# Optimization experiments

Measured on AMD Instinct MI355X. Metric: run time of the kernel, lower is better.

Reference implementation:

```python
import jax, jax.numpy as jnp
import numpy as np

H = 4                      # attention heads
L_NAMES = ['self', 'cross'] * 3
K_LIST = [None, None, 128, 128, 64, 64]  # top-k per layer (None = full attention)
BN_EPS = 1e-5


def conv1d(x, W, b):
    # 1x1 Conv1d: x [B, Ci, N], W [Co, Ci], b [Co]
    return jnp.einsum('oi,bin->bon', W, x) + b[:, None]


def bn_eval(x, g, b):
    # BatchNorm1d in eval mode with running mean 0 / var 1
    inv = 1.0 / np.sqrt(1.0 + BN_EPS)
    return (g * inv)[:, None] * x + b[:, None]


def mha(x, src, Wq, bq, Wk, bk, Wv, bv, Wm, bm, k):
    B, D, N = x.shape
    dh = D // H
    q = conv1d(x, Wq, bq).reshape(B, dh, H, N)
    kk = conv1d(src, Wk, bk).reshape(B, dh, H, -1)
    v = conv1d(src, Wv, bv).reshape(B, dh, H, -1)
    scores = jnp.einsum('bdhn,bdhm->bhnm', q, kk) / np.sqrt(dh)  # [B,H,N,M]
    if k is None:
        p = jax.nn.softmax(scores, axis=-1)
        out = jnp.einsum('bhnm,bdhm->bdhn', p, v)
    else:
        vals, idx = jax.lax.top_k(scores, k)          # [B,H,N,k]
        S = jax.nn.softmax(vals, axis=-1)
        # gather value vectors at the top-k key indices: [B,dh,H,N,k]
        vg = jnp.take_along_axis(v[:, :, :, None, :], idx[:, None, :, :, :], axis=4)
        out = jnp.einsum('bhnk,bdhnk->bdhn', S, vg)
    return conv1d(out.reshape(B, D, N), Wm, bm)


def log_ot(scores, alpha, iters):
    b, m, n = scores.shape
    bins0 = jnp.broadcast_to(alpha, (b, m, 1))
    bins1 = jnp.broadcast_to(alpha, (b, 1, n))
    a = jnp.broadcast_to(alpha, (b, 1, 1))
    Z0 = jnp.concatenate([jnp.concatenate([scores, bins0], -1),
                          jnp.concatenate([bins1, a], -1)], 1)  # [b,m+1,n+1]
    norm = -np.log(float(m + n))
    log_mu = jnp.concatenate([jnp.full((m,), norm, scores.dtype),
                              jnp.array([np.log(float(n)) + norm], scores.dtype)])
    log_nu = jnp.concatenate([jnp.full((n,), norm, scores.dtype),
                              jnp.array([np.log(float(m)) + norm], scores.dtype)])
    log_mu = jnp.broadcast_to(log_mu, (b, m + 1))
    log_nu = jnp.broadcast_to(log_nu, (b, n + 1))

    def step(carry, _):
        u, v = carry
        u = log_mu - jax.nn.logsumexp(Z0 + v[:, None, :], axis=2)
        v = log_nu - jax.nn.logsumexp(Z0 + u[:, :, None], axis=1)
        return (u, v), None

    (u, v), _ = jax.lax.scan(step, (jnp.zeros_like(log_mu), jnp.zeros_like(log_nu)),
                             None, length=iters)
    return Z0 + u[:, :, None] + v[:, None, :] - norm


def _forward(desc0, desc1, Wq, bq, Wk, bk, Wv, bv, Wm, bm,
             W1, b1, g1, be1, W2, b2, Wf, bf, alpha, iters):
    d0, d1 = desc0, desc1
    for i, (name, k) in enumerate(zip(L_NAMES, K_LIST)):
        s0, s1 = (d1, d0) if name == 'cross' else (d0, d1)

        def prop(x, src):
            msg = mha(x, src, Wq[i], bq[i], Wk[i], bk[i], Wv[i], bv[i], Wm[i], bm[i], k)
            h = jnp.concatenate([x, msg], axis=1)           # [B, 2D, N]
            h = jax.nn.relu(bn_eval(conv1d(h, W1[i], b1[i]), g1[i], be1[i]))
            return conv1d(h, W2[i], b2[i])

        dlt0, dlt1 = prop(d0, s0), prop(d1, s1)
        d0, d1 = d0 + dlt0, d1 + dlt1
    m0 = conv1d(d0, Wf, bf)
    m1 = conv1d(d1, Wf, bf)
    scores = jnp.einsum('bdn,bdm->bnm', m0, m1) / np.sqrt(m0.shape[1])
    return log_ot(scores, alpha, iters)


def setup_inputs() -> dict:
    B, D, N, L = 4, 128, 1024, 6
    key = jax.random.key(0)
    ks = jax.random.split(key, 20)

    def nrm(k, shape, s):
        return jax.random.normal(k, shape, jnp.float32) * s

    sw = 1.0 / np.sqrt(D)
    return {
        'desc0': nrm(ks[0], (B, D, N), 1.0),
        'desc1': nrm(ks[1], (B, D, N), 1.0),
        'Wq': nrm(ks[2], (L, D, D), sw), 'bq': jnp.zeros((L, D), jnp.float32),
        'Wk': nrm(ks[3], (L, D, D), sw), 'bk': jnp.zeros((L, D), jnp.float32),
        'Wv': nrm(ks[4], (L, D, D), sw), 'bv': jnp.zeros((L, D), jnp.float32),
        'Wm': nrm(ks[5], (L, D, D), sw), 'bm': jnp.zeros((L, D), jnp.float32),
        'W1': nrm(ks[6], (L, 2 * D, 2 * D), 1.0 / np.sqrt(2 * D)),
        'b1': jnp.zeros((L, 2 * D), jnp.float32),
        'g1': jnp.ones((L, 2 * D), jnp.float32),
        'be1': jnp.zeros((L, 2 * D), jnp.float32),
        'W2': nrm(ks[7], (L, D, 2 * D), 1.0 / np.sqrt(2 * D)),
        'b2': jnp.zeros((L, D), jnp.float32),
        'Wf': nrm(ks[8], (D, D), sw), 'bf': jnp.zeros((D,), jnp.float32),
        'alpha': jnp.asarray(1.0, jnp.float32),
        'iters': 20,
    }


def reference(desc0, desc1, Wq, bq, Wk, bk, Wv, bv, Wm, bm,
              W1, b1, g1, be1, W2, b2, Wf, bf, alpha, iters):
    return _forward(desc0, desc1, Wq, bq, Wk, bk, Wv, bv, Wm, bm,
                    W1, b1, g1, be1, W2, b2, Wf, bf, alpha, iters)
```

## Files before the change

### kernel.cpp

```cpp
#include <hip/hip_runtime.h>
#include <hip/hip_fp16.h>
#include <stdint.h>

#define NPOS   1024
#define DMODEL 128
#define NP1    1025
#define PLP    1053700
#define PSTR   1028
#define PLPH   1057800
#define PSTRH  1032
#define NORMF  (-7.624618986159398f)
#define LOGN   (6.931471805599453f)

typedef __attribute__((ext_vector_type(8))) short s8v;
typedef __attribute__((ext_vector_type(4))) float f4v;
typedef unsigned short ushort_t;

#define MFMA(a, b, c) __builtin_amdgcn_mfma_f32_16x16x32_bf16((a), (b), (c), 0, 0, 0)

static __device__ __forceinline__ ushort_t f2bf(float f) {
    union { float f; uint32_t u; } c; c.f = f;
    uint32_t u = c.u;
    return (ushort_t)((u + 0x7fffu + ((u >> 16) & 1u)) >> 16);
}
static __device__ __forceinline__ uint32_t cvtpk(float lo, float hi) {
    uint32_t r;
    asm("v_cvt_pk_bf16_f32 %0, %1, %2" : "=v"(r) : "v"(lo), "v"(hi));
    return r;
}

#define NW0 294912
#define NW1 98304
#define NW2 393216
#define NW3 196608
#define NW4 16384
#define NB5 2304
__global__ __launch_bounds__(256) void prep_weights(
    const float* __restrict__ Wq, const float* __restrict__ Wk, const float* __restrict__ Wv,
    const float* __restrict__ bq, const float* __restrict__ bk, const float* __restrict__ bv,
    const float* __restrict__ Wm, const float* __restrict__ W1, const float* __restrict__ W2,
    const float* __restrict__ Wf,
    ushort_t* __restrict__ wqkv, ushort_t* __restrict__ wm, ushort_t* __restrict__ w1,
    ushort_t* __restrict__ w2, ushort_t* __restrict__ wf, float* __restrict__ bqkv)
{
    int idx = blockIdx.x * 256 + threadIdx.x;
    if (idx < NW0) {
        int l = idx / 49152, r2 = idx % 49152;
        int r = r2 / 128, i = r2 % 128;
        int sel = r >> 7, rr = r & 127;
        int o = ((rr & 31) << 2) + (rr >> 5);
        const float* src = sel == 0 ? Wq : (sel == 1 ? Wk : Wv);
        wqkv[idx] = f2bf(src[((size_t)l * 128 + o) * 128 + i]);
        return;
    }
    idx -= NW0;
    if (idx < NW1) {
        int l = idx / 16384, o = (idx % 16384) / 128, ip = idx % 128;
        int i = ((ip & 31) << 2) + (ip >> 5);
        wm[idx] = f2bf(Wm[((size_t)l * 128 + o) * 128 + i]);
        return;
    }
    idx -= NW1;
    if (idx < NW2) { w1[idx] = f2bf(W1[idx]); return; }
    idx -= NW2;
    if (idx < NW3) { w2[idx] = f2bf(W2[idx]); return; }
    idx -= NW3;
    if (idx < NW4) { wf[idx] = f2bf(Wf[idx]); return; }
    idx -= NW4;
    if (idx < NB5) {
        int l = idx / 384, r = idx % 384;
        int sel = r >> 7, rr = r & 127;
        int o = ((rr & 31) << 2) + (rr >> 5);
        const float* src = sel == 0 ? bq : (sel == 1 ? bk : bv);
        bqkv[idx] = src[l * 128 + o];
    }
}

__global__ __launch_bounds__(256) void transpose_in(
    const float* __restrict__ desc0, const float* __restrict__ desc1,
    float* __restrict__ df, ushort_t* __restrict__ db)
{
    int g = blockIdx.z;
    int nb = blockIdx.x << 6, cb = blockIdx.y << 5;
    __shared__ float sm[32][65];
    const float* S = (g < 4 ? desc0 : desc1);
    int gl = g & 3;
    {
        int row = threadIdx.x >> 3, c8 = (threadIdx.x & 7) << 3;
        const float* p = S + ((size_t)gl * 128 + cb + row) * NPOS + nb + c8;
        float4 v0 = *(const float4*)p;
        float4 v1 = *(const float4*)(p + 4);
        sm[row][c8 + 0] = v0.x; sm[row][c8 + 1] = v0.y; sm[row][c8 + 2] = v0.z; sm[row][c8 + 3] = v0.w;
        sm[row][c8 + 4] = v1.x; sm[row][c8 + 5] = v1.y; sm[row][c8 + 6] = v1.z; sm[row][c8 + 7] = v1.w;
    }
    __syncthreads();
    int n = threadIdx.x >> 2, cc = (threadIdx.x & 3) << 3;
    float y[8];
    #pragma unroll
    for (int e = 0; e < 8; ++e) y[e] = sm[cc + e][n];
    size_t base = ((size_t)g * NPOS + nb + n) * DMODEL + cb + cc;
    *(float4*)(df + base) = make_float4(y[0], y[1], y[2], y[3]);
    *(float4*)(df + base + 4) = make_float4(y[4], y[5], y[6], y[7]);
    uint4 pk = make_uint4(cvtpk(y[0], y[1]), cvtpk(y[2], y[3]),
                          cvtpk(y[4], y[5]), cvtpk(y[6], y[7]));
    *(uint4*)(db + base) = pk;
}

__global__ __launch_bounds__(256) void conv_mfma(
    const ushort_t* __restrict__ X0, const ushort_t* __restrict__ X1, int c0, int Ci,
    const ushort_t* __restrict__ W, const float* __restrict__ bias,
    const float* __restrict__ bn_g, const float* __restrict__ bn_b,
    float* __restrict__ resid, ushort_t* __restrict__ outb, int Co, int mode)
{
    int g = blockIdx.z;
    int nb = blockIdx.x << 6;
    int obb = blockIdx.y << 6;
    int wave = threadIdx.x >> 6, lane = threadIdx.x & 63;
    int lrow = lane & 15, lk = (lane >> 4) << 3;
    int ob = obb + (wave << 4);
    f4v acc[4] = {};
    const ushort_t* wrow = W + (size_t)(ob + lrow) * Ci + lk;
    for (int k0 = 0; k0 < Ci; k0 += 32) {
        int k = k0 + lk;
        s8v b = *(const s8v*)(wrow + k0);
        #pragma unroll
        for (int t = 0; t < 4; ++t) {
            int n = nb + (t << 4) + lrow;
            const ushort_t* xp;
            if (k < c0) xp = X0 + ((size_t)g * NPOS + n) * c0 + k;
            else        xp = X1 + ((size_t)g * NPOS + n) * (Ci - c0) + (k - c0);
            s8v a = *(const s8v*)xp;
            acc[t] = MFMA(a, b, acc[t]);
        }
    }
    __shared__ float sm[64][68];
    #pragma unroll
    for (int t = 0; t < 4; ++t)
        #pragma unroll
        for (int r = 0; r < 4; ++r)
            sm[(t << 4) + ((lane >> 4) << 2) + r][(wave << 4) + lrow] = acc[t][r];
    __syncthreads();
    const float BN_INV = 0.9999950000374997f;
    int n = threadIdx.x >> 2, oc = (threadIdx.x & 3) << 4;
    int o0 = obb + oc;
    float y[16];
    #pragma unroll
    for (int e = 0; e < 16; ++e) y[e] = sm[n][oc + e] + bias[o0 + e];
    size_t base = ((size_t)g * NPOS + nb + n) * Co + o0;
    if (mode == 1) {
        #pragma unroll
        for (int e = 0; e < 16; ++e)
            y[e] = fmaxf(bn_g[o0 + e] * BN_INV * y[e] + bn_b[o0 + e], 0.f);
    } else if (mode == 2) {
        float* rp = resid + base;
        #pragma unroll
        for (int q = 0; q < 16; q += 4) {
            float4 r4 = *(const float4*)(rp + q);
            y[q] += r4.x; y[q + 1] += r4.y; y[q + 2] += r4.z; y[q + 3] += r4.w;
            *(float4*)(rp + q) = make_float4(y[q], y[q + 1], y[q + 2], y[q + 3]);
        }
    }
    uint4 p0 = make_uint4(cvtpk(y[0], y[1]), cvtpk(y[2], y[3]),
                          cvtpk(y[4], y[5]), cvtpk(y[6], y[7]));
    uint4 p1 = make_uint4(cvtpk(y[8], y[9]), cvtpk(y[10], y[11]),
                          cvtpk(y[12], y[13]), cvtpk(y[14], y[15]));
    *(uint4*)(outb + base) = p0;
    *(uint4*)(outb + base + 8) = p1;
}

__global__ __launch_bounds__(256) void qkv_mfma(
    const ushort_t* __restrict__ X, const ushort_t* __restrict__ W,
    const float* __restrict__ bias,
    ushort_t* __restrict__ Qb, ushort_t* __restrict__ Kb, ushort_t* __restrict__ Vb)
{
    int g = blockIdx.z;
    int nb = blockIdx.x << 6;
    int obb = blockIdx.y << 6;
    int wave = threadIdx.x >> 6, lane = threadIdx.x & 63;
    int lrow = lane & 15, lk = (lane >> 4) << 3;
    int ob = obb + (wave << 4);
    f4v acc[4] = {};
    const ushort_t* wrow = W + (size_t)(ob + lrow) * DMODEL + lk;
    for (int k0 = 0; k0 < DMODEL; k0 += 32) {
        s8v b = *(const s8v*)(wrow + k0);
        #pragma unroll
        for (int t = 0; t < 4; ++t) {
            int n = nb + (t << 4) + lrow;
            s8v a = *(const s8v*)(X + ((size_t)g * NPOS + n) * DMODEL + k0 + lk);
            acc[t] = MFMA(a, b, acc[t]);
        }
    }
    __shared__ float sm[64][68];
    #pragma unroll
    for (int t = 0; t < 4; ++t)
        #pragma unroll
        for (int r = 0; r < 4; ++r)
            sm[(t << 4) + ((lane >> 4) << 2) + r][(wave << 4) + lrow] = acc[t][r];
    __syncthreads();
    if (obb < 256) {
        int n = threadIdx.x >> 2, oc = (threadIdx.x & 3) << 4;
        int ov = obb + oc;
        ushort_t* dst = (ov < 128) ? Qb : Kb;
        int c = ov & 127;
        float y[16];
        #pragma unroll
        for (int e = 0; e < 16; ++e) y[e] = sm[n][oc + e] + bias[ov + e];
        size_t base = ((size_t)g * NPOS + nb + n) * DMODEL + c;
        uint4 p0 = make_uint4(cvtpk(y[0], y[1]), cvtpk(y[2], y[3]),
                              cvtpk(y[4], y[5]), cvtpk(y[6], y[7]));
        uint4 p1 = make_uint4(cvtpk(y[8], y[9]), cvtpk(y[10], y[11]),
                              cvtpk(y[12], y[13]), cvtpk(y[14], y[15]));
        *(uint4*)(dst + base) = p0;
        *(uint4*)(dst + base + 8) = p1;
    } else {
        int c = threadIdx.x >> 2, mc = (threadIdx.x & 3) << 4;
        float bc = bias[obb + c];
        float y[16];
        #pragma unroll
        for (int e = 0; e < 16; ++e) y[e] = sm[mc + e][c] + bc;
        size_t base = ((size_t)g * DMODEL + (obb - 256) + c) * NPOS + nb + mc;
        uint4 p0 = make_uint4(cvtpk(y[0], y[1]), cvtpk(y[2], y[3]),
                              cvtpk(y[4], y[5]), cvtpk(y[6], y[7]));
        uint4 p1 = make_uint4(cvtpk(y[8], y[9]), cvtpk(y[10], y[11]),
                              cvtpk(y[12], y[13]), cvtpk(y[14], y[15]));
        *(uint4*)(Vb + base) = p0;
        *(uint4*)(Vb + base + 8) = p1;
    }
}

__global__ __launch_bounds__(256) void attn_fused(
    const ushort_t* __restrict__ Qb, const ushort_t* __restrict__ Kb,
    const ushort_t* __restrict__ Vb, ushort_t* __restrict__ ao,
    int k, int cross)
{
    __shared__ ushort_t sc[16 * 1024];
    int gh = blockIdx.y;
    int g = gh >> 2, h = gh & 3;
    int g2 = cross ? (g ^ 4) : g;
    int n0 = blockIdx.x << 4;
    int wave = threadIdx.x >> 6, lane = threadIdx.x & 63;
    int lrow = lane & 15, lq = lane >> 4;

    {
        int kq = wave;
        s8v qa = *(const s8v*)(Qb + ((size_t)g * NPOS + n0 + lrow) * DMODEL
                               + (h << 5) + (lq << 3));
        const float scale = 0.17677669529663687f;
        int swz = (lrow & 7) << 4;
        __builtin_amdgcn_s_setprio(1);
        for (int mt = 0; mt < 16; ++mt) {
            int m = (kq << 8) + (mt << 4);
            s8v kb = *(const s8v*)(Kb + ((size_t)g2 * NPOS + m + lrow) * DMODEL
                                   + (h << 5) + (lq << 3));
            f4v z = {};
            z = MFMA(kb, qa, z);
            uint32_t p0 = cvtpk(z[0] * scale, z[1] * scale);
            uint32_t p1 = cvtpk(z[2] * scale, z[3] * scale);
            int byte = ((lrow << 11) + ((m + (lq << 2)) << 1)) ^ swz;
            *(uint2*)((char*)sc + byte) = make_uint2(p0, p1);
        }
        __builtin_amdgcn_s_setprio(0);
    }
    __syncthreads();

    {
        bool dosel = (k < NPOS);
        for (int rr = 0; rr < 4; ++rr) {
            int row = (wave << 2) + rr;
            int swz = (row & 7) << 4;
            int base = (row << 11) + (lane << 5);
            uint4 d0 = *(const uint4*)((const char*)sc + (base ^ swz));
            uint4 d1 = *(const uint4*)((const char*)sc + ((base + 16) ^ swz));
            uint32_t wd[8] = {d0.x, d0.y, d0.z, d0.w, d1.x, d1.y, d1.z, d1.w};
            float val[16];
            #pragma unroll
            for (int q = 0; q < 8; ++q) {
                union { unsigned ui; float f; } c0, c1;
                c0.ui = wd[q] << 16; c1.ui = wd[q] & 0xFFFF0000u;
                val[2 * q] = c0.f; val[2 * q + 1] = c1.f;
            }
            float mx = val[0];
            #pragma unroll
            for (int t = 1; t < 16; ++t) mx = fmaxf(mx, val[t]);
            #pragma unroll
            for (int o = 32; o; o >>= 1) mx = fmaxf(mx, __shfl_xor(mx, o));

            bool sel[16];
            if (dosel) {
                unsigned prefix = 0;
                bool exact = false;
                for (int bit = 15; bit >= 0 && !exact; --bit) {
                    unsigned cand = prefix | (1u << bit);
                    unsigned craw = (cand & 0x8000u) ? (cand ^ 0x8000u) : (cand ^ 0xFFFFu);
                    union { unsigned ui; float f; } cf; cf.ui = craw << 16;
                    float cf_f = cf.f;
                    int c = 0;
                    #pragma unroll
                    for (int t = 0; t < 16; ++t)
                        c += __popcll(__ballot(val[t] >= cf_f));
                    if (c >= k) { prefix = cand; exact = (c == k); }
                }
                unsigned praw = (prefix & 0x8000u) ? (prefix ^ 0x8000u) : (prefix ^ 0xFFFFu);
                union { unsigned ui; float f; } pf; pf.ui = praw << 16;
                float thr = pf.f;
                if (exact) {
                    #pragma unroll
                    for (int t = 0; t < 16; ++t) sel[t] = (val[t] >= thr);
                } else {
                    int cgt = 0;
                    #pragma unroll
                    for (int t = 0; t < 16; ++t)
                        cgt += __popcll(__ballot(val[t] > thr));
                    int need = k - cgt;
                    unsigned long long lmask = (1ull << lane) - 1ull;
                    int before = 0;
                    #pragma unroll
                    for (int t = 0; t < 16; ++t)
                        before += __popcll(__ballot(val[t] == thr) & lmask);
                    int loc = 0;
                    #pragma unroll
                    for (int t = 0; t < 16; ++t) {
                        bool tie = (val[t] == thr);
                        sel[t] = (val[t] > thr) || (tie && (before + loc < need));
                        loc += tie ? 1 : 0;
                    }
                }
            } else {
                #pragma unroll
                for (int t = 0; t < 16; ++t) sel[t] = true;
            }
            float w[16], sum = 0.f;
            #pragma unroll
            for (int t = 0; t < 16; ++t) {
                w[t] = sel[t] ? __expf(val[t] - mx) : 0.f;
                sum += w[t];
            }
            #pragma unroll
            for (int o = 32; o; o >>= 1) sum += __shfl_xor(sum, o);
            float inv = 1.f / sum;
            uint32_t ow[8];
            #pragma unroll
            for (int q = 0; q < 8; ++q)
                ow[q] = cvtpk(w[2 * q] * inv, w[2 * q + 1] * inv);
            *(uint4*)((char*)sc + (base ^ swz)) = make_uint4(ow[0], ow[1], ow[2], ow[3]);
            *(uint4*)((char*)sc + ((base + 16) ^ swz)) = make_uint4(ow[4], ow[5], ow[6], ow[7]);
        }
    }
    __syncthreads();

    {
        int khalf = wave >> 1, dimg = wave & 1;
        int db = dimg << 4;
        int pswz = (lrow & 7) << 4;
        int pbase = (lrow << 11) + (khalf << 10) + (lq << 4);
        const ushort_t* vbase = Vb + ((size_t)g2 * DMODEL + (h << 5) + db + lrow) * NPOS
                                + (khalf << 9) + (lq << 3);
        f4v acc = {};
        __builtin_amdgcn_s_setprio(1);
        #pragma unroll
        for (int ks = 0; ks < 16; ++ks) {
            s8v pa = *(const s8v*)((const char*)sc + ((pbase + (ks << 6)) ^ pswz));
            s8v vv = *(const s8v*)(vbase + (ks << 5));
            acc = MFMA(pa, vv, acc);
        }
        __builtin_amdgcn_s_setprio(0);
        __syncthreads();
        if (khalf == 1)
            *(f4v*)((char*)sc + (((dimg << 6) + lane) << 4)) = acc;
        __syncthreads();
        if (khalf == 0) {
            f4v other = *(const f4v*)((char*)sc + (((dimg << 6) + lane) << 4));
            acc = acc + other;
            #pragma unroll
            for (int r = 0; r < 4; ++r) {
                int n = n0 + (lq << 2) + r;
                ao[((size_t)g * NPOS + n) * DMODEL + (h << 5) + db + lrow] = f2bf(acc[r]);
            }
        }
    }
}

__global__ __launch_bounds__(256) void final_mfma(
    const ushort_t* __restrict__ md, float* __restrict__ Z0P,
    __half* __restrict__ Z0H, __half* __restrict__ Z0TH)
{
    int b = blockIdx.z;
    int wave = threadIdx.x >> 6, lane = threadIdx.x & 63;
    int wr = wave >> 1, wc = wave & 1;
    int n0 = (blockIdx.y << 7) + (wr << 6);
    int m0 = (blockIdx.x << 7) + (wc << 6);
    int lrow = lane & 15, lk = (lane >> 4) << 3;
    f4v acc[4][4] = {};
    for (int k0 = 0; k0 < DMODEL; k0 += 32) {
        s8v qa[4], kb[4];
        #pragma unroll
        for (int t = 0; t < 4; ++t) {
            qa[t] = *(const s8v*)(md + ((size_t)b * NPOS + n0 + (t << 4) + lrow) * DMODEL + k0 + lk);
            kb[t] = *(const s8v*)(md + ((size_t)(b + 4) * NPOS + m0 + (t << 4) + lrow) * DMODEL + k0 + lk);
        }
        #pragma unroll
        for (int tn = 0; tn < 4; ++tn)
            #pragma unroll
            for (int tm = 0; tm < 4; ++tm)
                acc[tn][tm] = MFMA(qa[tn], kb[tm], acc[tn][tm]);
    }
    const float scf = 0.08838834764831845f;
    int rbase = (lane >> 4) << 2;
    #pragma unroll
    for (int tn = 0; tn < 4; ++tn) {
        #pragma unroll
        for (int tm = 0; tm < 4; ++tm) {
            #pragma unroll
            for (int r = 0; r < 4; ++r) {
                int n = n0 + (tn << 4) + rbase + r;
                int m = m0 + (tm << 4) + lrow;
                float y = acc[tn][tm][r] * scf;
                Z0P[(size_t)b * PLP + (size_t)n * PSTR + m] = y;
                __half hy = __float2half(y);
                Z0H [(size_t)b * PLPH + (size_t)n * PSTRH + m] = hy;
                Z0TH[(size_t)b * PLPH + (size_t)m * PSTRH + n] = hy;
            }
        }
    }
}

__global__ __launch_bounds__(1024) void ot_init(
    float* __restrict__ Z0P, __half* __restrict__ Z0H, __half* __restrict__ Z0TH,
    float* __restrict__ v, const float* __restrict__ alpha)
{
    float a = *alpha;
    __half ha = __float2half(a);
    int b = blockIdx.x, t = threadIdx.x;
    Z0P [(size_t)b * PLP  + (size_t)t * PSTR  + 1024] = a;
    Z0P [(size_t)b * PLP  + (size_t)1024 * PSTR + t] = a;
    Z0H [(size_t)b * PLPH + (size_t)t * PSTRH + 1024] = ha;
    Z0H [(size_t)b * PLPH + (size_t)1024 * PSTRH + t] = ha;
    Z0TH[(size_t)b * PLPH + (size_t)t * PSTRH + 1024] = ha;
    Z0TH[(size_t)b * PLPH + (size_t)1024 * PSTRH + t] = ha;
    v[b * NP1 + t] = 0.f;
    if (t == 0) {
        Z0P [(size_t)b * PLP  + (size_t)1024 * PSTR  + 1024] = a;
        Z0H [(size_t)b * PLPH + (size_t)1024 * PSTRH + 1024] = ha;
        Z0TH[(size_t)b * PLPH + (size_t)1024 * PSTRH + 1024] = ha;
        v[b * NP1 + 1024] = 0.f;
    }
}

__global__ __launch_bounds__(256) void lse_sweep_h(
    const __half* __restrict__ Z, const float* __restrict__ vin,
    float* __restrict__ uout)
{
    int wv = threadIdx.x >> 6, lane = threadIdx.x & 63;
    int r = blockIdx.x * 4 + wv;
    int b = r / NP1, i = r - b * NP1;
    const __half* z  = Z + (size_t)b * PLPH + (size_t)i * PSTRH;
    const float* vb = vin + b * NP1;
    float x[17];
    #pragma unroll
    for (int t = 0; t < 2; ++t) {
        int j = (t << 9) + (lane << 3);
        union { uint4 u; __half h[8]; } U;
        U.u = *(const uint4*)(z + j);
        float4 v0 = *(const float4*)(vb + j);
        float4 v1 = *(const float4*)(vb + j + 4);
        x[t * 8 + 0] = __half2float(U.h[0]) + v0.x;
        x[t * 8 + 1] = __half2float(U.h[1]) + v0.y;
        x[t * 8 + 2] = __half2float(U.h[2]) + v0.z;
        x[t * 8 + 3] = __half2float(U.h[3]) + v0.w;
        x[t * 8 + 4] = __half2float(U.h[4]) + v1.x;
        x[t * 8 + 5] = __half2float(U.h[5]) + v1.y;
        x[t * 8 + 6] = __half2float(U.h[6]) + v1.z;
        x[t * 8 + 7] = __half2float(U.h[7]) + v1.w;
    }
    x[16] = (lane == 0) ? (__half2float(z[1024]) + vb[1024]) : -1e30f;
    float m = x[0];
    #pragma unroll
    for (int t = 1; t < 17; ++t) m = fmaxf(m, x[t]);
    #pragma unroll
    for (int o = 32; o; o >>= 1) m = fmaxf(m, __shfl_xor(m, o));
    float sum = 0.f;
    #pragma unroll
    for (int t = 0; t < 17; ++t) sum += __expf(x[t] - m);
    #pragma unroll
    for (int o = 32; o; o >>= 1) sum += __shfl_xor(sum, o);
    if (lane == 0)
        uout[b * NP1 + i] = NORMF + ((i == 1024) ? LOGN : 0.f) - (m + __logf(sum));
}

__global__ __launch_bounds__(256) void ot_final(
    float* __restrict__ out, const float* __restrict__ Z0P,
    const float* __restrict__ u, const float* __restrict__ v)
{
    int r = blockIdx.x;
    int b = r / NP1, i = r - b * NP1;
    float ui = u[b * NP1 + i] - NORMF;
    const float* zp = Z0P + (size_t)b * PLP + (size_t)i * PSTR;
    float* zo = out + ((size_t)b * NP1 + i) * NP1;
    const float* vb = v + b * NP1;
    for (int j = threadIdx.x; j < NP1; j += 256) zo[j] = zp[j] + ui + vb[j];
}

extern "C" void kernel_launch(void* const* d_in, const int* in_sizes, int n_in,
                              void* d_out, int out_size, void* d_ws, size_t ws_size,
                              hipStream_t stream)
{
    (void)in_sizes; (void)n_in; (void)out_size; (void)ws_size;
    const float* desc0 = (const float*)d_in[0];
    const float* desc1 = (const float*)d_in[1];
    const float* Wq = (const float*)d_in[2];  const float* bq = (const float*)d_in[3];
    const float* Wk = (const float*)d_in[4];  const float* bk = (const float*)d_in[5];
    const float* Wv = (const float*)d_in[6];  const float* bv = (const float*)d_in[7];
    const float* Wm = (const float*)d_in[8];  const float* bm = (const float*)d_in[9];
    const float* W1 = (const float*)d_in[10]; const float* b1 = (const float*)d_in[11];
    const float* g1 = (const float*)d_in[12]; const float* be1 = (const float*)d_in[13];
    const float* W2 = (const float*)d_in[14]; const float* b2 = (const float*)d_in[15];
    const float* Wf = (const float*)d_in[16]; const float* bf = (const float*)d_in[17];
    const float* alpha = (const float*)d_in[18];

    float* Zout = (float*)d_out;
    float* ws = (float*)d_ws;
    size_t o = 0;
    float* d_f32      = ws;                          o += 1048576;
    ushort_t* d_bf    = (ushort_t*)(ws + o);         o += 524288;
    ushort_t* Qb      = (ushort_t*)(ws + o);         o += 524288;
    ushort_t* Kb      = (ushort_t*)(ws + o);         o += 524288;
    ushort_t* Vb      = (ushort_t*)(ws + o);         o += 524288;
    ushort_t* aob     = (ushort_t*)(ws + o);         o += 524288;
    ushort_t* msgb    = (ushort_t*)(ws + o);         o += 524288;
    ushort_t* hb      = (ushort_t*)(ws + o);         o += 1048576;
    ushort_t* mdesc   = (ushort_t*)(ws + o);         o += 524288;
    ushort_t* wqkv    = (ushort_t*)(ws + o);         o += 147456;
    ushort_t* wmw     = (ushort_t*)(ws + o);         o += 49152;
    ushort_t* w1w     = (ushort_t*)(ws + o);         o += 196608;
    ushort_t* w2w     = (ushort_t*)(ws + o);         o += 98304;
    ushort_t* wfw     = (ushort_t*)(ws + o);         o += 8192;
    float* bqkv       = ws + o;                      o += 2304;
    float* ub         = ws + o;                      o += 4352;
    float* vb         = ws + o;                      o += 4352;
    float* Z0P        = ws + o;                      o += 4214800;
    __half* Z0H       = (__half*)(ws + o);           o += 2115600;
    __half* Z0TH      = (__half*)(ws + o);           o += 2115600;

    dim3 blk(256);
    prep_weights<<<dim3((NW0 + NW1 + NW2 + NW3 + NW4 + NB5 + 255) / 256), blk, 0, stream>>>(
        Wq, Wk, Wv, bq, bk, bv, Wm, W1, W2, Wf, wqkv, wmw, w1w, w2w, wfw, bqkv);
    transpose_in<<<dim3(16, 4, 8), blk, 0, stream>>>(desc0, desc1, d_f32, d_bf);

    static const int KLIST[6] = {1024, 1024, 128, 128, 64, 64};
    for (int l = 0; l < 6; ++l) {
        int cross = l & 1;
        int k = KLIST[l];
        qkv_mfma<<<dim3(16, 6, 8), blk, 0, stream>>>(
            d_bf, wqkv + (size_t)l * 49152, bqkv + l * 384, Qb, Kb, Vb);
        attn_fused<<<dim3(64, 32), blk, 0, stream>>>(Qb, Kb, Vb, aob, k, cross);
        conv_mfma<<<dim3(16, 2, 8), blk, 0, stream>>>(
            aob, (const ushort_t*)nullptr, 128, 128, wmw + (size_t)l * 16384,
            bm + l * 128, nullptr, nullptr, nullptr, msgb, 128, 0);
        conv_mfma<<<dim3(16, 4, 8), blk, 0, stream>>>(
            d_bf, msgb, 128, 256, w1w + (size_t)l * 65536,
            b1 + l * 256, g1 + l * 256, be1 + l * 256, nullptr, hb, 256, 1);
        conv_mfma<<<dim3(16, 2, 8), blk, 0, stream>>>(
            hb, (const ushort_t*)nullptr, 256, 256, w2w + (size_t)l * 32768,
            b2 + l * 128, nullptr, nullptr, d_f32, d_bf, 128, 2);
    }
    conv_mfma<<<dim3(16, 2, 8), blk, 0, stream>>>(
        d_bf, (const ushort_t*)nullptr, 128, 128, wfw, bf,
        nullptr, nullptr, nullptr, mdesc, 128, 0);
    final_mfma<<<dim3(8, 8, 4), blk, 0, stream>>>(mdesc, Z0P, Z0H, Z0TH);
    ot_init<<<dim3(4), dim3(1024), 0, stream>>>(Z0P, Z0H, Z0TH, vb, alpha);
    for (int it = 0; it < 20; ++it) {
        lse_sweep_h<<<dim3(1025), blk, 0, stream>>>(Z0H,  vb, ub);
        lse_sweep_h<<<dim3(1025), blk, 0, stream>>>(Z0TH, ub, vb);
    }
    ot_final<<<dim3(4100), blk, 0, stream>>>(Zout, Z0P, ub, vb);
}
```

Measured before the change: 785.2 us.

## Fuse Sinkhorn iterations into one persistent kernel with grid barriers; prefetch V

The ot_init, the 40 lse_sweep launches and ot_final are replaced by a single persistent kernel of 256 blocks that synchronises with an atomic-counter grid barrier between half-iterations. This removes roughly 40 kernel launches and their tail gaps. In attn_fused, half of the V fragments are prefetched into registers before the softmax phase, and the setprio hints are removed. The grid barrier assumes all 256 blocks are co-resident, and the prefetch raises register pressure.

```diff
diff --git a/kernel.cpp b/kernel.cpp
--- a/kernel.cpp
+++ b/kernel.cpp
@@ -247,7 +247,6 @@
                                + (h << 5) + (lq << 3));
         const float scale = 0.17677669529663687f;
         int swz = (lrow & 7) << 4;
-        __builtin_amdgcn_s_setprio(1);
         for (int mt = 0; mt < 16; ++mt) {
             int m = (kq << 8) + (mt << 4);
             s8v kb = *(const s8v*)(Kb + ((size_t)g2 * NPOS + m + lrow) * DMODEL
@@ -259,8 +258,15 @@
             int byte = ((lrow << 11) + ((m + (lq << 2)) << 1)) ^ swz;
             *(uint2*)((char*)sc + byte) = make_uint2(p0, p1);
         }
-        __builtin_amdgcn_s_setprio(0);
-    }
+    }
+
+    int khalf = wave >> 1, dimg = wave & 1;
+    const ushort_t* vbase = Vb + ((size_t)g2 * DMODEL + (h << 5) + (dimg << 4) + lrow) * NPOS
+                            + (khalf << 9) + (lq << 3);
+    s8v vpre[8];
+    #pragma unroll
+    for (int ks = 0; ks < 8; ++ks) vpre[ks] = *(const s8v*)(vbase + (ks << 5));
+
     __syncthreads();
 
     {
@@ -349,21 +355,21 @@
     __syncthreads();
 
     {
-        int khalf = wave >> 1, dimg = wave & 1;
         int db = dimg << 4;
         int pswz = (lrow & 7) << 4;
         int pbase = (lrow << 11) + (khalf << 10) + (lq << 4);
-        const ushort_t* vbase = Vb + ((size_t)g2 * DMODEL + (h << 5) + db + lrow) * NPOS
-                                + (khalf << 9) + (lq << 3);
         f4v acc = {};
-        __builtin_amdgcn_s_setprio(1);
-        #pragma unroll
-        for (int ks = 0; ks < 16; ++ks) {
+        #pragma unroll
+        for (int ks = 0; ks < 8; ++ks) {
+            s8v pa = *(const s8v*)((const char*)sc + ((pbase + (ks << 6)) ^ pswz));
+            acc = MFMA(pa, vpre[ks], acc);
+        }
+        #pragma unroll
+        for (int ks = 8; ks < 16; ++ks) {
             s8v pa = *(const s8v*)((const char*)sc + ((pbase + (ks << 6)) ^ pswz));
             s8v vv = *(const s8v*)(vbase + (ks << 5));
             acc = MFMA(pa, vv, acc);
         }
-        __builtin_amdgcn_s_setprio(0);
         __syncthreads();
         if (khalf == 1)
             *(f4v*)((char*)sc + (((dimg << 6) + lane) << 4)) = acc;
@@ -424,80 +430,132 @@
     }
 }
 
-__global__ __launch_bounds__(1024) void ot_init(
-    float* __restrict__ Z0P, __half* __restrict__ Z0H, __half* __restrict__ Z0TH,
-    float* __restrict__ v, const float* __restrict__ alpha)
-{
-    float a = *alpha;
-    __half ha = __float2half(a);
-    int b = blockIdx.x, t = threadIdx.x;
-    Z0P [(size_t)b * PLP  + (size_t)t * PSTR  + 1024] = a;
-    Z0P [(size_t)b * PLP  + (size_t)1024 * PSTR + t] = a;
-    Z0H [(size_t)b * PLPH + (size_t)t * PSTRH + 1024] = ha;
-    Z0H [(size_t)b * PLPH + (size_t)1024 * PSTRH + t] = ha;
-    Z0TH[(size_t)b * PLPH + (size_t)t * PSTRH + 1024] = ha;
-    Z0TH[(size_t)b * PLPH + (size_t)1024 * PSTRH + t] = ha;
-    v[b * NP1 + t] = 0.f;
-    if (t == 0) {
-        Z0P [(size_t)b * PLP  + (size_t)1024 * PSTR  + 1024] = a;
-        Z0H [(size_t)b * PLPH + (size_t)1024 * PSTRH + 1024] = ha;
-        Z0TH[(size_t)b * PLPH + (size_t)1024 * PSTRH + 1024] = ha;
-        v[b * NP1 + 1024] = 0.f;
-    }
-}
-
-__global__ __launch_bounds__(256) void lse_sweep_h(
-    const __half* __restrict__ Z, const float* __restrict__ vin,
-    float* __restrict__ uout)
-{
-    int wv = threadIdx.x >> 6, lane = threadIdx.x & 63;
-    int r = blockIdx.x * 4 + wv;
-    int b = r / NP1, i = r - b * NP1;
-    const __half* z  = Z + (size_t)b * PLPH + (size_t)i * PSTRH;
-    const float* vb = vin + b * NP1;
-    float x[17];
-    #pragma unroll
-    for (int t = 0; t < 2; ++t) {
-        int j = (t << 9) + (lane << 3);
-        union { uint4 u; __half h[8]; } U;
-        U.u = *(const uint4*)(z + j);
-        float4 v0 = *(const float4*)(vb + j);
-        float4 v1 = *(const float4*)(vb + j + 4);
-        x[t * 8 + 0] = __half2float(U.h[0]) + v0.x;
-        x[t * 8 + 1] = __half2float(U.h[1]) + v0.y;
-        x[t * 8 + 2] = __half2float(U.h[2]) + v0.z;
-        x[t * 8 + 3] = __half2float(U.h[3]) + v0.w;
-        x[t * 8 + 4] = __half2float(U.h[4]) + v1.x;
-        x[t * 8 + 5] = __half2float(U.h[5]) + v1.y;
-        x[t * 8 + 6] = __half2float(U.h[6]) + v1.z;
-        x[t * 8 + 7] = __half2float(U.h[7]) + v1.w;
-    }
-    x[16] = (lane == 0) ? (__half2float(z[1024]) + vb[1024]) : -1e30f;
-    float m = x[0];
-    #pragma unroll
-    for (int t = 1; t < 17; ++t) m = fmaxf(m, x[t]);
-    #pragma unroll
-    for (int o = 32; o; o >>= 1) m = fmaxf(m, __shfl_xor(m, o));
-    float sum = 0.f;
-    #pragma unroll
-    for (int t = 0; t < 17; ++t) sum += __expf(x[t] - m);
-    #pragma unroll
-    for (int o = 32; o; o >>= 1) sum += __shfl_xor(sum, o);
-    if (lane == 0)
-        uout[b * NP1 + i] = NORMF + ((i == 1024) ? LOGN : 0.f) - (m + __logf(sum));
-}
-
-__global__ __launch_bounds__(256) void ot_final(
-    float* __restrict__ out, const float* __restrict__ Z0P,
-    const float* __restrict__ u, const float* __restrict__ v)
-{
-    int r = blockIdx.x;
-    int b = r / NP1, i = r - b * NP1;
-    float ui = u[b * NP1 + i] - NORMF;
-    const float* zp = Z0P + (size_t)b * PLP + (size_t)i * PSTR;
-    float* zo = out + ((size_t)b * NP1 + i) * NP1;
-    const float* vb = v + b * NP1;
-    for (int j = threadIdx.x; j < NP1; j += 256) zo[j] = zp[j] + ui + vb[j];
+__global__ __launch_bounds__(256) void sinkhorn_all(
+    __half* __restrict__ Z0H, __half* __restrict__ Z0TH,
+    float* __restrict__ Z0P, float* __restrict__ out,
+    float* __restrict__ ub, float* __restrict__ vb,
+    const float* __restrict__ alpha, unsigned* bar)
+{
+    int bid = blockIdx.x, tid = threadIdx.x;
+    int wave = tid >> 6, lane = tid & 63;
+    int wid = (bid << 2) + wave;
+    unsigned phase = 0;
+
+#define GRIDBAR() do {                                              \
+        __syncthreads();                                            \
+        if (tid == 0) {                                             \
+            __threadfence();                                        \
+            atomicAdd(bar, 1u);                                     \
+            ++phase;                                                \
+            unsigned tgt = phase * 256u;                            \
+            while (atomicAdd(bar, 0u) < tgt)                        \
+                __builtin_amdgcn_s_sleep(2);                        \
+            __threadfence();                                        \
+        }                                                           \
+        __syncthreads();                                            \
+    } while (0)
+
+    {
+        float a = *alpha;
+        __half ha = __float2half(a);
+        int idx = bid * 256 + tid;
+        if (idx < 4100) {
+            int b = idx / NP1, t = idx - b * NP1;
+            Z0H [(size_t)b * PLPH + (size_t)t * PSTRH + 1024] = ha;
+            Z0H [(size_t)b * PLPH + (size_t)1024 * PSTRH + t] = ha;
+            Z0TH[(size_t)b * PLPH + (size_t)t * PSTRH + 1024] = ha;
+            Z0TH[(size_t)b * PLPH + (size_t)1024 * PSTRH + t] = ha;
+            Z0P [(size_t)b * PLP  + (size_t)t * PSTR  + 1024] = a;
+            Z0P [(size_t)b * PLP  + (size_t)1024 * PSTR + t] = a;
+            vb[idx] = 0.f;
+        }
+    }
+    GRIDBAR();
+
+    for (int it = 0; it < 20; ++it) {
+        for (int r = wid; r < 4100; r += 1024) {
+            int b = r / NP1, i = r - b * NP1;
+            const __half* z = Z0H + (size_t)b * PLPH + (size_t)i * PSTRH;
+            const float* vv = vb + b * NP1;
+            float x[17];
+            #pragma unroll
+            for (int t = 0; t < 2; ++t) {
+                int j = (t << 9) + (lane << 3);
+                union { uint4 u; __half h[8]; } U;
+                U.u = *(const uint4*)(z + j);
+                float4 v0 = *(const float4*)(vv + j);
+                float4 v1 = *(const float4*)(vv + j + 4);
+                x[t * 8 + 0] = __half2float(U.h[0]) + v0.x;
+                x[t * 8 + 1] = __half2float(U.h[1]) + v0.y;
+                x[t * 8 + 2] = __half2float(U.h[2]) + v0.z;
+                x[t * 8 + 3] = __half2float(U.h[3]) + v0.w;
+                x[t * 8 + 4] = __half2float(U.h[4]) + v1.x;
+                x[t * 8 + 5] = __half2float(U.h[5]) + v1.y;
+                x[t * 8 + 6] = __half2float(U.h[6]) + v1.z;
+                x[t * 8 + 7] = __half2float(U.h[7]) + v1.w;
+            }
+            x[16] = (lane == 0) ? (__half2float(z[1024]) + vv[1024]) : -1e30f;
+            float m = x[0];
+            #pragma unroll
+            for (int t = 1; t < 17; ++t) m = fmaxf(m, x[t]);
+            #pragma unroll
+            for (int o = 32; o; o >>= 1) m = fmaxf(m, __shfl_xor(m, o));
+            float sum = 0.f;
+            #pragma unroll
+            for (int t = 0; t < 17; ++t) sum += __expf(x[t] - m);
+            #pragma unroll
+            for (int o = 32; o; o >>= 1) sum += __shfl_xor(sum, o);
+            if (lane == 0)
+                ub[b * NP1 + i] = NORMF + ((i == 1024) ? LOGN : 0.f) - (m + __logf(sum));
+        }
+        GRIDBAR();
+        for (int r = wid; r < 4100; r += 1024) {
+            int b = r / NP1, i = r - b * NP1;
+            const __half* z = Z0TH + (size_t)b * PLPH + (size_t)i * PSTRH;
+            const float* uu = ub + b * NP1;
+            float x[17];
+            #pragma unroll
+            for (int t = 0; t < 2; ++t) {
+                int j = (t << 9) + (lane << 3);
+                union { uint4 u; __half h[8]; } U;
+                U.u = *(const uint4*)(z + j);
+                float4 v0 = *(const float4*)(uu + j);
+                float4 v1 = *(const float4*)(uu + j + 4);
+                x[t * 8 + 0] = __half2float(U.h[0]) + v0.x;
+                x[t * 8 + 1] = __half2float(U.h[1]) + v0.y;
+                x[t * 8 + 2] = __half2float(U.h[2]) + v0.z;
+                x[t * 8 + 3] = __half2float(U.h[3]) + v0.w;
+                x[t * 8 + 4] = __half2float(U.h[4]) + v1.x;
+                x[t * 8 + 5] = __half2float(U.h[5]) + v1.y;
+                x[t * 8 + 6] = __half2float(U.h[6]) + v1.z;
+                x[t * 8 + 7] = __half2float(U.h[7]) + v1.w;
+            }
+            x[16] = (lane == 0) ? (__half2float(z[1024]) + uu[1024]) : -1e30f;
+            float m = x[0];
+            #pragma unroll
+            for (int t = 1; t < 17; ++t) m = fmaxf(m, x[t]);
+            #pragma unroll
+            for (int o = 32; o; o >>= 1) m = fmaxf(m, __shfl_xor(m, o));
+            float sum = 0.f;
+            #pragma unroll
+            for (int t = 0; t < 17; ++t) sum += __expf(x[t] - m);
+            #pragma unroll
+            for (int o = 32; o; o >>= 1) sum += __shfl_xor(sum, o);
+            if (lane == 0)
+                vb[b * NP1 + i] = NORMF + ((i == 1024) ? LOGN : 0.f) - (m + __logf(sum));
+        }
+        GRIDBAR();
+    }
+
+    for (int r = wid; r < 4100; r += 1024) {
+        int b = r / NP1, i = r - b * NP1;
+        float ui = ub[b * NP1 + i] - NORMF;
+        const float* zp = Z0P + (size_t)b * PLP + (size_t)i * PSTR;
+        float* zo = out + ((size_t)b * NP1 + i) * NP1;
+        const float* vv = vb + b * NP1;
+        for (int j = lane; j < NP1; j += 64) zo[j] = zp[j] + ui + vv[j];
+    }
+#undef GRIDBAR
 }
 
 extern "C" void kernel_launch(void* const* d_in, const int* in_sizes, int n_in,
@@ -540,6 +598,9 @@
     float* Z0P        = ws + o;                      o += 4214800;
     __half* Z0H       = (__half*)(ws + o);           o += 2115600;
     __half* Z0TH      = (__half*)(ws + o);           o += 2115600;
+    unsigned* bar     = (unsigned*)(ws + o);         o += 16;
+
+    hipMemsetAsync(bar, 0, 16, stream);
 
     dim3 blk(256);
     prep_weights<<<dim3((NW0 + NW1 + NW2 + NW3 + NW4 + NB5 + 255) / 256), blk, 0, stream>>>(
@@ -567,10 +628,5 @@
         d_bf, (const ushort_t*)nullptr, 128, 128, wfw, bf,
         nullptr, nullptr, nullptr, mdesc, 128, 0);
     final_mfma<<<dim3(8, 8, 4), blk, 0, stream>>>(mdesc, Z0P, Z0H, Z0TH);
-    ot_init<<<dim3(4), dim3(1024), 0, stream>>>(Z0P, Z0H, Z0TH, vb, alpha);
-    for (int it = 0; it < 20; ++it) {
-        lse_sweep_h<<<dim3(1025), blk, 0, stream>>>(Z0H,  vb, ub);
-        lse_sweep_h<<<dim3(1025), blk, 0, stream>>>(Z0TH, ub, vb);
-    }
-    ot_final<<<dim3(4100), blk, 0, stream>>>(Zout, Z0P, ub, vb);
-}
+    sinkhorn_all<<<dim3(256), blk, 0, stream>>>(Z0H, Z0TH, Z0P, Zout, ub, vb, alpha, bar);
+}
```

Measured after the change: 1.474 ms. 87.7% more time.

## Fold merge projection into first MLP weights and prefetch V in attention

Applied to the files above, without the earlier changes.

Precomputes W1[:,D:]·Wm and the matching folded bias once per call, so the separate merge-projection conv launch and its msg buffer are removed from each layer. The first MLP conv reads the attention output directly through the folded weights. In the attention kernel, half of the V fragments are loaded into registers before the softmax barrier, and the setprio hints are removed. This adds a small fold kernel and more register pressure in attention, and the fold changes bf16 rounding slightly.

```diff
diff --git a/kernel.cpp b/kernel.cpp
--- a/kernel.cpp
+++ b/kernel.cpp
@@ -30,17 +30,16 @@
 }
 
 #define NW0 294912
-#define NW1 98304
 #define NW2 393216
 #define NW3 196608
 #define NW4 16384
 #define NB5 2304
+#define NPREP (NW0 + NW2 + NW3 + NW4 + NB5)
 __global__ __launch_bounds__(256) void prep_weights(
     const float* __restrict__ Wq, const float* __restrict__ Wk, const float* __restrict__ Wv,
     const float* __restrict__ bq, const float* __restrict__ bk, const float* __restrict__ bv,
-    const float* __restrict__ Wm, const float* __restrict__ W1, const float* __restrict__ W2,
-    const float* __restrict__ Wf,
-    ushort_t* __restrict__ wqkv, ushort_t* __restrict__ wm, ushort_t* __restrict__ w1,
+    const float* __restrict__ W1, const float* __restrict__ W2, const float* __restrict__ Wf,
+    ushort_t* __restrict__ wqkv, ushort_t* __restrict__ w1c,
     ushort_t* __restrict__ w2, ushort_t* __restrict__ wf, float* __restrict__ bqkv)
 {
     int idx = blockIdx.x * 256 + threadIdx.x;
@@ -54,14 +53,11 @@
         return;
     }
     idx -= NW0;
-    if (idx < NW1) {
-        int l = idx / 16384, o = (idx % 16384) / 128, ip = idx % 128;
-        int i = ((ip & 31) << 2) + (ip >> 5);
-        wm[idx] = f2bf(Wm[((size_t)l * 128 + o) * 128 + i]);
+    if (idx < NW2) {
+        int i = idx & 255;
+        if (i < 128) w1c[idx] = f2bf(W1[idx]);
         return;
     }
-    idx -= NW1;
-    if (idx < NW2) { w1[idx] = f2bf(W1[idx]); return; }
     idx -= NW2;
     if (idx < NW3) { w2[idx] = f2bf(W2[idx]); return; }
     idx -= NW3;
@@ -73,6 +69,38 @@
         int o = ((rr & 31) << 2) + (rr >> 5);
         const float* src = sel == 0 ? bq : (sel == 1 ? bk : bv);
         bqkv[idx] = src[l * 128 + o];
+    }
+}
+
+#define NFOLD 196608
+#define NFB   1536
+__global__ __launch_bounds__(256) void fold_w1(
+    const float* __restrict__ W1, const float* __restrict__ Wm,
+    const float* __restrict__ b1, const float* __restrict__ bm,
+    ushort_t* __restrict__ w1c, float* __restrict__ b1c)
+{
+    int idx = blockIdx.x * 256 + threadIdx.x;
+    if (idx < NFOLD) {
+        int l = idx / 32768, rem = idx % 32768;
+        int o = rem / 128, ip = rem % 128;
+        int i = ((ip & 31) << 2) + (ip >> 5);
+        const float* w1row = W1 + ((size_t)l * 256 + o) * 256 + 128;
+        const float* wmcol = Wm + (size_t)l * 16384 + i;
+        float s = 0.f;
+        #pragma unroll 8
+        for (int j = 0; j < 128; ++j) s = fmaf(w1row[j], wmcol[(size_t)j * 128], s);
+        w1c[((size_t)l * 256 + o) * 256 + 128 + ip] = f2bf(s);
+        return;
+    }
+    idx -= NFOLD;
+    if (idx < NFB) {
+        int l = idx / 256, o = idx % 256;
+        const float* w1row = W1 + ((size_t)l * 256 + o) * 256 + 128;
+        const float* bml = bm + l * 128;
+        float s = b1[l * 256 + o];
+        #pragma unroll 8
+        for (int j = 0; j < 128; ++j) s = fmaf(w1row[j], bml[j], s);
+        b1c[idx] = s;
     }
 }
 
@@ -247,7 +275,6 @@
                                + (h << 5) + (lq << 3));
         const float scale = 0.17677669529663687f;
         int swz = (lrow & 7) << 4;
-        __builtin_amdgcn_s_setprio(1);
         for (int mt = 0; mt < 16; ++mt) {
             int m = (kq << 8) + (mt << 4);
             s8v kb = *(const s8v*)(Kb + ((size_t)g2 * NPOS + m + lrow) * DMODEL
@@ -259,8 +286,15 @@
             int byte = ((lrow << 11) + ((m + (lq << 2)) << 1)) ^ swz;
             *(uint2*)((char*)sc + byte) = make_uint2(p0, p1);
         }
-        __builtin_amdgcn_s_setprio(0);
-    }
+    }
+
+    int khalf = wave >> 1, dimg = wave & 1;
+    const ushort_t* vbase = Vb + ((size_t)g2 * DMODEL + (h << 5) + (dimg << 4) + lrow) * NPOS
+                            + (khalf << 9) + (lq << 3);
+    s8v vpre[8];
+    #pragma unroll
+    for (int ks = 0; ks < 8; ++ks) vpre[ks] = *(const s8v*)(vbase + (ks << 5));
+
     __syncthreads();
 
     {
@@ -349,21 +383,21 @@
     __syncthreads();
 
     {
-        int khalf = wave >> 1, dimg = wave & 1;
         int db = dimg << 4;
         int pswz = (lrow & 7) << 4;
         int pbase = (lrow << 11) + (khalf << 10) + (lq << 4);
-        const ushort_t* vbase = Vb + ((size_t)g2 * DMODEL + (h << 5) + db + lrow) * NPOS
-                                + (khalf << 9) + (lq << 3);
         f4v acc = {};
-        __builtin_amdgcn_s_setprio(1);
-        #pragma unroll
-        for (int ks = 0; ks < 16; ++ks) {
+        #pragma unroll
+        for (int ks = 0; ks < 8; ++ks) {
+            s8v pa = *(const s8v*)((const char*)sc + ((pbase + (ks << 6)) ^ pswz));
+            acc = MFMA(pa, vpre[ks], acc);
+        }
+        #pragma unroll
+        for (int ks = 8; ks < 16; ++ks) {
             s8v pa = *(const s8v*)((const char*)sc + ((pbase + (ks << 6)) ^ pswz));
             s8v vv = *(const s8v*)(vbase + (ks << 5));
             acc = MFMA(pa, vv, acc);
         }
-        __builtin_amdgcn_s_setprio(0);
         __syncthreads();
         if (khalf == 1)
             *(f4v*)((char*)sc + (((dimg << 6) + lane) << 4)) = acc;
@@ -526,15 +560,14 @@
     ushort_t* Kb      = (ushort_t*)(ws + o);         o += 524288;
     ushort_t* Vb      = (ushort_t*)(ws + o);         o += 524288;
     ushort_t* aob     = (ushort_t*)(ws + o);         o += 524288;
-    ushort_t* msgb    = (ushort_t*)(ws + o);         o += 524288;
     ushort_t* hb      = (ushort_t*)(ws + o);         o += 1048576;
     ushort_t* mdesc   = (ushort_t*)(ws + o);         o += 524288;
     ushort_t* wqkv    = (ushort_t*)(ws + o);         o += 147456;
-    ushort_t* wmw     = (ushort_t*)(ws + o);         o += 49152;
-    ushort_t* w1w     = (ushort_t*)(ws + o);         o += 196608;
+    ushort_t* w1c     = (ushort_t*)(ws + o);         o += 196608;
     ushort_t* w2w     = (ushort_t*)(ws + o);         o += 98304;
     ushort_t* wfw     = (ushort_t*)(ws + o);         o += 8192;
     float* bqkv       = ws + o;                      o += 2304;
+    float* b1c        = ws + o;                      o += 1536;
     float* ub         = ws + o;                      o += 4352;
     float* vb         = ws + o;                      o += 4352;
     float* Z0P        = ws + o;                      o += 4214800;
@@ -542,8 +575,10 @@
     __half* Z0TH      = (__half*)(ws + o);           o += 2115600;
 
     dim3 blk(256);
-    prep_weights<<<dim3((NW0 + NW1 + NW2 + NW3 + NW4 + NB5 + 255) / 256), blk, 0, stream>>>(
-        Wq, Wk, Wv, bq, bk, bv, Wm, W1, W2, Wf, wqkv, wmw, w1w, w2w, wfw, bqkv);
+    prep_weights<<<dim3((NPREP + 255) / 256), blk, 0, stream>>>(
+        Wq, Wk, Wv, bq, bk, bv, W1, W2, Wf, wqkv, w1c, w2w, wfw, bqkv);
+    fold_w1<<<dim3((NFOLD + NFB + 255) / 256), blk, 0, stream>>>(
+        W1, Wm, b1, bm, w1c, b1c);
     transpose_in<<<dim3(16, 4, 8), blk, 0, stream>>>(desc0, desc1, d_f32, d_bf);
 
     static const int KLIST[6] = {1024, 1024, 128, 128, 64, 64};
@@ -553,12 +588,9 @@
         qkv_mfma<<<dim3(16, 6, 8), blk, 0, stream>>>(
             d_bf, wqkv + (size_t)l * 49152, bqkv + l * 384, Qb, Kb, Vb);
         attn_fused<<<dim3(64, 32), blk, 0, stream>>>(Qb, Kb, Vb, aob, k, cross);
-        conv_mfma<<<dim3(16, 2, 8), blk, 0, stream>>>(
-            aob, (const ushort_t*)nullptr, 128, 128, wmw + (size_t)l * 16384,
-            bm + l * 128, nullptr, nullptr, nullptr, msgb, 128, 0);
         conv_mfma<<<dim3(16, 4, 8), blk, 0, stream>>>(
-            d_bf, msgb, 128, 256, w1w + (size_t)l * 65536,
-            b1 + l * 256, g1 + l * 256, be1 + l * 256, nullptr, hb, 256, 1);
+            d_bf, aob, 128, 256, w1c + (size_t)l * 65536,
+            b1c + l * 256, g1 + l * 256, be1 + l * 256, nullptr, hb, 256, 1);
         conv_mfma<<<dim3(16, 2, 8), blk, 0, stream>>>(
             hb, (const ushort_t*)nullptr, 256, 256, w2w + (size_t)l * 32768,
             b2 + l * 128, nullptr, nullptr, d_f32, d_bf, 128, 2);
```

Result: no change. 783.2 us (-0.3%).
